# Kernel optimization log

Measured on AMD Instinct MI355X. Metric: run time of the kernel, lower is better.

The kernel has to match this reference:

```python
import jax, jax.numpy as jnp
import numpy as np

B, Cin, H, W = 4, 64, 160, 160
Cout, K, STRIDE, PAD = 64, 3, 1, 1
KK = K * K


def setup_inputs() -> dict:
    key = jax.random.key(0)
    ks = jax.random.split(key, 4)
    x = jax.random.normal(ks[0], (B, Cin, H, W), jnp.float32)
    # offset/mask conv params (zero-init in source; small random so offsets are non-trivial)
    offset_w = jax.random.normal(ks[1], (3 * KK, Cin, K, K), jnp.float32) * 0.01
    offset_b = jax.random.normal(ks[2], (3 * KK,), jnp.float32) * 0.01
    fan_in = Cin * K * K
    weight = jax.random.normal(ks[3], (Cout, Cin, K, K), jnp.float32) / np.sqrt(fan_in)
    bias = jnp.zeros((Cout,), jnp.float32)
    return dict(x=x, offset_w=offset_w, offset_b=offset_b, weight=weight, bias=bias)


def _conv2d(x, w, b):
    y = jax.lax.conv_general_dilated(
        x, w, window_strides=(STRIDE, STRIDE),
        padding=[(PAD, PAD), (PAD, PAD)],
        dimension_numbers=('NCHW', 'OIHW', 'NCHW'))
    return y + b[None, :, None, None]


def _deform_conv2d(x, offset, mask, weight, bias):
    # x: [B,C,H,W]; offset: [B,2*KK,Ho,Wo] as (dy,dx) pairs; mask: [B,KK,Ho,Wo]
    Bs, C, Hh, Ww = x.shape
    Ho, Wo = offset.shape[2], offset.shape[3]
    off = offset.reshape(Bs, KK, 2, Ho, Wo)
    dy, dx = off[:, :, 0], off[:, :, 1]            # [B,KK,Ho,Wo]
    ki, kj = jnp.meshgrid(jnp.arange(K), jnp.arange(K), indexing='ij')
    ki = ki.reshape(KK).astype(jnp.float32)
    kj = kj.reshape(KK).astype(jnp.float32)
    hb = (jnp.arange(Ho) * STRIDE - PAD).astype(jnp.float32)
    wb = (jnp.arange(Wo) * STRIDE - PAD).astype(jnp.float32)
    py = dy + ki[None, :, None, None] + hb[None, None, :, None]  # sample y coords
    px = dx + kj[None, :, None, None] + wb[None, None, None, :]  # sample x coords
    y0 = jnp.floor(py); x0 = jnp.floor(px)
    wy1 = py - y0; wy0 = 1.0 - wy1
    wx1 = px - x0; wx0 = 1.0 - wx1
    x_hwc = jnp.transpose(x, (0, 2, 3, 1))          # [B,H,W,C]

    def corner(yc, xc):
        valid = (yc >= 0) & (yc < Hh) & (xc >= 0) & (xc < Ww)
        yi = jnp.clip(yc, 0, Hh - 1).astype(jnp.int32)
        xi = jnp.clip(xc, 0, Ww - 1).astype(jnp.int32)
        g = jax.vmap(lambda img, yy, xx: img[yy, xx])(x_hwc, yi, xi)  # [B,KK,Ho,Wo,C]
        return g * valid[..., None].astype(x.dtype)

    val = (corner(y0, x0) * (wy0 * wx0)[..., None]
           + corner(y0, x0 + 1.0) * (wy0 * wx1)[..., None]
           + corner(y0 + 1.0, x0) * (wy1 * wx0)[..., None]
           + corner(y0 + 1.0, x0 + 1.0) * (wy1 * wx1)[..., None])
    val = val * mask[..., None]                      # modulated (DCNv2)
    w2 = weight.reshape(weight.shape[0], C, KK)      # [O,C,KK]
    out = jnp.einsum('bkhwc,ock->bohw', val, w2)
    return out + bias[None, :, None, None]


def reference(x, offset_w, offset_b, weight, bias):
    out = _conv2d(x, offset_w, offset_b)             # [B,3*KK,Ho,Wo]
    o1, o2, m = jnp.split(out, 3, axis=1)
    offset = jnp.concatenate([o1, o2], axis=1)       # [B,2*KK,Ho,Wo]
    mask = jax.nn.sigmoid(m)
    return _deform_conv2d(x, offset, mask, weight, bias)
```

## Files before the change

### kernel.cpp

```cpp
#include <hip/hip_runtime.h>
#include <hip/hip_bf16.h>
#include <math.h>

#define B_ 4
#define CIN 64
#define H_ 160
#define W_ 160
#define COUT 64
#define KK_ 9
#define HW_ (H_ * W_)
#define KTOT 576
#define APITCH 584
#define XPITCH 72
#define SLPITCH 17
#define NTILE 6400
#define TPX   800

typedef __attribute__((ext_vector_type(8))) short bf16x8;
typedef __attribute__((ext_vector_type(4))) float f32x4;

__device__ inline unsigned short f2bf(float f) {
    unsigned int u = __float_as_uint(f);
    u = (u + 0x7FFF + ((u >> 16) & 1)) >> 16;
    return (unsigned short)u;
}

__device__ inline unsigned short bfc(float f) {
    __hip_bfloat16 h = __float2bfloat16(f);
    union { __hip_bfloat16 h; unsigned short u; } cv;
    cv.h = h;
    return cv.u;
}

__global__ __launch_bounds__(256) void prep_all_k(const float* __restrict__ x,
                                                  const float* __restrict__ wgt,
                                                  const float* __restrict__ ow,
                                                  float* __restrict__ xt,
                                                  unsigned short* __restrict__ wB,
                                                  unsigned short* __restrict__ wB2) {
    __shared__ float tile[64][65];
    int bid = blockIdx.x;
    int t = threadIdx.x;

    if (bid < 1600) {
        int pbk = bid % 400, b = bid / 400;
        int p0 = pbk * 64;
        const float* xp = x + (size_t)b * CIN * HW_ + p0;

        int pg = (t & 15) * 4, cr = t >> 4;
#pragma unroll
        for (int i = 0; i < 4; i++) {
            int c = i * 16 + cr;
            float4 v = *(const float4*)(xp + (size_t)c * HW_ + pg);
            tile[c][pg]     = v.x;
            tile[c][pg + 1] = v.y;
            tile[c][pg + 2] = v.z;
            tile[c][pg + 3] = v.w;
        }
        __syncthreads();

        int c4 = (t & 15) * 4, pr = t >> 4;
        float* op = xt + ((size_t)b * HW_ + p0) * 64 + c4;
#pragma unroll
        for (int i = 0; i < 4; i++) {
            int p = i * 16 + pr;
            float4 v;
            v.x = tile[c4][p];
            v.y = tile[c4 + 1][p];
            v.z = tile[c4 + 2][p];
            v.w = tile[c4 + 3][p];
            *(float4*)(op + (size_t)p * 64) = v;
        }
    } else if (bid < 1744) {
        int i = (bid - 1600) * 256 + t;
        int o = i / KTOT, r = i % KTOT;
        int tap = r >> 6, c = r & 63;
        wB[i] = f2bf(wgt[(o * CIN + c) * KK_ + tap]);
    } else {
        int i = (bid - 1744) * 256 + t;
        int n = i / KTOT, r = i % KTOT;
        int tap = r >> 6, c = r & 63;
        wB2[i] = (n < 27) ? f2bf(ow[(n * CIN + c) * KK_ + tap]) : (unsigned short)0;
    }
}

__global__ __launch_bounds__(256, 6) void fused_dcn_k(const float* __restrict__ xt,
                                                      const unsigned short* __restrict__ wB2,
                                                      const float* __restrict__ ob,
                                                      const unsigned short* __restrict__ wB,
                                                      const float* __restrict__ bias,
                                                      float* __restrict__ out) {
    __shared__ __align__(16) char ubuf[16 * APITCH * 2];
    __shared__ __align__(16) char pbuf[144 * 32];
    __shared__ float slog[27 * SLPITCH];
    unsigned short* sX = (unsigned short*)ubuf;
    unsigned short* sA = (unsigned short*)ubuf;
    float4* spar_w = (float4*)pbuf;
    int4*   spar_o = (int4*)(pbuf + 144 * 16);

    int t = threadIdx.x;
    int lane = t & 63, wv = t >> 6;
    int bid = blockIdx.x;
    int tile = (bid & 7) * TPX + (bid >> 3);
    int gp0 = tile * 16;
    int wo0 = gp0 % W_;
    int tmp = gp0 / W_;
    int ho = tmp % H_;
    int b  = tmp / H_;

    const float* xb = xt + (size_t)b * HW_ * 64 + lane;

    for (int i = 0; i < 14; i++) {
        int r = i * 4 + wv;
        if (r < 54) {
            int yy = ho - 1 + r / 18;
            int xx = wo0 - 1 + r % 18;
            float v = 0.f;
            if (yy >= 0 && yy < H_ && xx >= 0 && xx < W_)
                v = xb[(size_t)(yy * W_ + xx) * 64];
            sX[r * XPITCH + lane] = bfc(v);
        }
    }
    __syncthreads();

    if (wv < 2) {
        int m = lane & 15, q = lane >> 4;
        int oc = wv * 16 + m;
        float bv = (oc < 27) ? ob[oc] : 0.f;
        f32x4 acc  = {bv, bv, bv, bv};
        f32x4 acc2 = {0.f, 0.f, 0.f, 0.f};
        const unsigned short* brow = wB2 + oc * KTOT + q * 8;
#pragma unroll
        for (int tap = 0; tap < 9; tap++) {
            int row = (tap / 3) * 18 + (tap % 3) + m;
            const unsigned short* sxr = sX + row * XPITCH + q * 8;
            bf16x8 af0 = *(const bf16x8*)(sxr);
            bf16x8 af1 = *(const bf16x8*)(sxr + 32);
            bf16x8 b0  = *(const bf16x8*)(brow + (2 * tap) * 32);
            bf16x8 b1  = *(const bf16x8*)(brow + (2 * tap + 1) * 32);
            acc  = __builtin_amdgcn_mfma_f32_16x16x32_bf16(af0, b0, acc,  0, 0, 0);
            acc2 = __builtin_amdgcn_mfma_f32_16x16x32_bf16(af1, b1, acc2, 0, 0, 0);
        }
#pragma unroll
        for (int r = 0; r < 4; r++) acc[r] += acc2[r];
        if (oc < 27) {
            float* sl = slog + oc * SLPITCH + q * 4;
            if (oc < 18) {
#pragma unroll
                for (int r = 0; r < 4; r++) sl[r] = acc[r];
            } else {
#pragma unroll
                for (int r = 0; r < 4; r++) sl[r] = 1.f / (1.f + expf(-acc[r]));
            }
        }
    }
    __syncthreads();

    if (lane < 36) {
        int task = lane * 4 + wv;
        int p = task & 15, k = task >> 4;
        float dyv = slog[(2 * k) * SLPITCH + p];
        float dxv = slog[(2 * k + 1) * SLPITCH + p];
        float mv  = slog[(18 + k) * SLPITCH + p];
        float py = dyv + (float)(k / 3) + (float)(ho - 1);
        float px = dxv + (float)(k % 3) + (float)(wo0 + p - 1);
        float y0f = floorf(py), x0f = floorf(px);
        float wy1 = py - y0f, wx1 = px - x0f;
        float wy0 = 1.f - wy1, wx0 = 1.f - wx1;
        int y0 = (int)y0f, x0 = (int)x0f;
        bool yv0 = (y0 >= 0) && (y0 < H_);
        bool yv1 = (y0 + 1 >= 0) && (y0 + 1 < H_);
        bool xv0 = (x0 >= 0) && (x0 < W_);
        bool xv1 = (x0 + 1 >= 0) && (x0 + 1 < W_);
        float4 w4;
        w4.x = (yv0 && xv0) ? wy0 * wx0 * mv : 0.f;
        w4.y = (yv0 && xv1) ? wy0 * wx1 * mv : 0.f;
        w4.z = (yv1 && xv0) ? wy1 * wx0 * mv : 0.f;
        w4.w = (yv1 && xv1) ? wy1 * wx1 * mv : 0.f;
        spar_w[task] = w4;
        int yc0 = min(max(y0, 0), H_ - 1), yc1 = min(max(y0 + 1, 0), H_ - 1);
        int xc0 = min(max(x0, 0), W_ - 1), xc1 = min(max(x0 + 1, 0), W_ - 1);
        int4 o4;
        o4.x = (yc0 * W_ + xc0) * 256;
        o4.y = (yc0 * W_ + xc1) * 256;
        o4.z = (yc1 * W_ + xc0) * 256;
        o4.w = (yc1 * W_ + xc1) * 256;
        spar_o[task] = o4;
    }
    __asm__ volatile("s_waitcnt lgkmcnt(0)" ::: "memory");

    {
        unsigned lane4 = (unsigned)lane << 2;
        const char* xu = (const char*)xt + (size_t)b * ((size_t)HW_ * 64 * 4);
#pragma unroll
        for (int g = 0; g < 6; g++) {
            float v00[6], v01[6], v10[6], v11[6];
#pragma unroll
            for (int j = 0; j < 6; j++) {
                int task = (g * 6 + j) * 4 + wv;
                int4 o4 = spar_o[task];
                v00[j] = *(const float*)(xu + ((unsigned)o4.x + lane4));
                v01[j] = *(const float*)(xu + ((unsigned)o4.y + lane4));
                v10[j] = *(const float*)(xu + ((unsigned)o4.z + lane4));
                v11[j] = *(const float*)(xu + ((unsigned)o4.w + lane4));
            }
#pragma unroll
            for (int j = 0; j < 6; j++) {
                int task = (g * 6 + j) * 4 + wv;
                float4 w4 = spar_w[task];
                int p = task & 15, k = task >> 4;
                float v = v00[j] * w4.x + v01[j] * w4.y
                        + v10[j] * w4.z + v11[j] * w4.w;
                sA[p * APITCH + k * 64 + lane] = bfc(v);
            }
        }
    }
    __syncthreads();

    int m = lane & 15, q = lane >> 4;
    int o0 = wv * 16 + m;
    float b0v = bias[o0];
    f32x4 acc0 = {b0v, b0v, b0v, b0v};
    f32x4 acc1 = {0.f, 0.f, 0.f, 0.f};
    const unsigned short* arow = sA + m * APITCH + q * 8;
    const unsigned short* br0 = wB + o0 * KTOT + q * 8;
#pragma unroll
    for (int tap = 0; tap < 9; tap++) {
        bf16x8 af0 = *(const bf16x8*)(arow + (2 * tap) * 32);
        bf16x8 af1 = *(const bf16x8*)(arow + (2 * tap + 1) * 32);
        bf16x8 b0  = *(const bf16x8*)(br0 + (2 * tap) * 32);
        bf16x8 b1  = *(const bf16x8*)(br0 + (2 * tap + 1) * 32);
        acc0 = __builtin_amdgcn_mfma_f32_16x16x32_bf16(af0, b0, acc0, 0, 0, 0);
        acc1 = __builtin_amdgcn_mfma_f32_16x16x32_bf16(af1, b1, acc1, 0, 0, 0);
    }
#pragma unroll
    for (int r = 0; r < 4; r++) acc0[r] += acc1[r];

    size_t a0 = ((size_t)(b * COUT + o0)) * HW_ + (size_t)ho * W_ + wo0 + q * 4;
    float4 r0; r0.x = acc0[0]; r0.y = acc0[1]; r0.z = acc0[2]; r0.w = acc0[3];
    *(float4*)(out + a0) = r0;
}

extern "C" void kernel_launch(void* const* d_in, const int* in_sizes, int n_in,
                              void* d_out, int out_size, void* d_ws, size_t ws_size,
                              hipStream_t stream) {
    const float* x    = (const float*)d_in[0];
    const float* ow   = (const float*)d_in[1];
    const float* ob   = (const float*)d_in[2];
    const float* wgt  = (const float*)d_in[3];
    const float* bias = (const float*)d_in[4];
    float* out = (float*)d_out;

    float* ws  = (float*)d_ws;
    float* xt  = ws;
    unsigned short* wB  = (unsigned short*)(xt + (size_t)B_ * HW_ * CIN);
    unsigned short* wB2 = wB + (size_t)COUT * KTOT;

    prep_all_k<<<1816, 256, 0, stream>>>(x, wgt, ow, xt, wB, wB2);
    fused_dcn_k<<<NTILE, 256, 0, stream>>>(xt, wB2, ob, wB, bias, out);
}
```

Measured before the change: 200.6 us.

## Stage a 5x20 fp32 input halo in LDS and gather bilinear corners from it

Each block loads a 5-row by 20-column fp32 halo of the input (all 64 channels) into shared memory and uses it to build the bf16 tile for the offset conv. Bilinear sample corners that fall inside this halo are read from LDS, and only out-of-window samples fall back to global gathers, flagged per task. The aim is to replace scattered global gathers with LDS reads, since offsets are small. In exchange, LDS use per block grows by about 25 KB and the launch-bounds occupancy hint drops from 6 to 3 blocks.

```diff
diff --git a/kernel.cpp b/kernel.cpp
--- a/kernel.cpp
+++ b/kernel.cpp
@@ -84,7 +84,7 @@
     }
 }
 
-__global__ __launch_bounds__(256, 6) void fused_dcn_k(const float* __restrict__ xt,
+__global__ __launch_bounds__(256, 3) void fused_dcn_k(const float* __restrict__ xt,
                                                       const unsigned short* __restrict__ wB2,
                                                       const float* __restrict__ ob,
                                                       const unsigned short* __restrict__ wB,
@@ -93,6 +93,8 @@
     __shared__ __align__(16) char ubuf[16 * APITCH * 2];
     __shared__ __align__(16) char pbuf[144 * 32];
     __shared__ float slog[27 * SLPITCH];
+    __shared__ unsigned sflag[144];
+    __shared__ __align__(16) float sF[100 * 64];
     unsigned short* sX = (unsigned short*)ubuf;
     unsigned short* sA = (unsigned short*)ubuf;
     float4* spar_w = (float4*)pbuf;
@@ -110,16 +112,18 @@
 
     const float* xb = xt + (size_t)b * HW_ * 64 + lane;
 
-    for (int i = 0; i < 14; i++) {
-        int r = i * 4 + wv;
-        if (r < 54) {
-            int yy = ho - 1 + r / 18;
-            int xx = wo0 - 1 + r % 18;
-            float v = 0.f;
-            if (yy >= 0 && yy < H_ && xx >= 0 && xx < W_)
-                v = xb[(size_t)(yy * W_ + xx) * 64];
-            sX[r * XPITCH + lane] = bfc(v);
-        }
+#pragma unroll
+    for (int i = 0; i < 25; i++) {
+        int p = i * 4 + wv;
+        int ry = p / 20, rx = p % 20;
+        int yy = ho - 2 + ry;
+        int xx = wo0 - 2 + rx;
+        float v = 0.f;
+        if (yy >= 0 && yy < H_ && xx >= 0 && xx < W_)
+            v = xb[(size_t)(yy * W_ + xx) * 64];
+        sF[p * 64 + lane] = v;
+        if (ry >= 1 && ry <= 3 && rx >= 1 && rx <= 18)
+            sX[((ry - 1) * 18 + (rx - 1)) * XPITCH + lane] = bfc(v);
     }
     __syncthreads();
 
@@ -180,38 +184,77 @@
         spar_w[task] = w4;
         int yc0 = min(max(y0, 0), H_ - 1), yc1 = min(max(y0 + 1, 0), H_ - 1);
         int xc0 = min(max(x0, 0), W_ - 1), xc1 = min(max(x0 + 1, 0), W_ - 1);
+        bool ins = (yc0 >= ho - 2) && (yc1 <= ho + 2) &&
+                   (xc0 >= wo0 - 2) && (xc1 <= wo0 + 17);
         int4 o4;
-        o4.x = (yc0 * W_ + xc0) * 256;
-        o4.y = (yc0 * W_ + xc1) * 256;
-        o4.z = (yc1 * W_ + xc0) * 256;
-        o4.w = (yc1 * W_ + xc1) * 256;
+        if (ins) {
+            int ry0 = yc0 - (ho - 2), ry1 = yc1 - (ho - 2);
+            int rx0 = xc0 - (wo0 - 2), rx1 = xc1 - (wo0 - 2);
+            o4.x = (ry0 * 20 + rx0) * 256;
+            o4.y = (ry0 * 20 + rx1) * 256;
+            o4.z = (ry1 * 20 + rx0) * 256;
+            o4.w = (ry1 * 20 + rx1) * 256;
+        } else {
+            o4.x = (yc0 * W_ + xc0) * 256;
+            o4.y = (yc0 * W_ + xc1) * 256;
+            o4.z = (yc1 * W_ + xc0) * 256;
+            o4.w = (yc1 * W_ + xc1) * 256;
+        }
         spar_o[task] = o4;
+        sflag[task] = ins ? 0u : 1u;
     }
     __asm__ volatile("s_waitcnt lgkmcnt(0)" ::: "memory");
 
     {
         unsigned lane4 = (unsigned)lane << 2;
-        const char* xu = (const char*)xt + (size_t)b * ((size_t)HW_ * 64 * 4);
+        const char* xu  = (const char*)xt + (size_t)b * ((size_t)HW_ * 64 * 4);
+        const char* sFb = (const char*)sF;
 #pragma unroll
         for (int g = 0; g < 6; g++) {
-            float v00[6], v01[6], v10[6], v11[6];
+            int4 o4[6]; float4 w4[6]; unsigned fl = 0;
 #pragma unroll
             for (int j = 0; j < 6; j++) {
                 int task = (g * 6 + j) * 4 + wv;
-                int4 o4 = spar_o[task];
-                v00[j] = *(const float*)(xu + ((unsigned)o4.x + lane4));
-                v01[j] = *(const float*)(xu + ((unsigned)o4.y + lane4));
-                v10[j] = *(const float*)(xu + ((unsigned)o4.z + lane4));
-                v11[j] = *(const float*)(xu + ((unsigned)o4.w + lane4));
+                o4[j] = spar_o[task];
+                w4[j] = spar_w[task];
+                fl |= sflag[task];
+            }
+            float v[6];
+            if (fl == 0) {
+#pragma unroll
+                for (int j = 0; j < 6; j++) {
+                    float v00 = *(const float*)(sFb + ((unsigned)o4[j].x + lane4));
+                    float v01 = *(const float*)(sFb + ((unsigned)o4[j].y + lane4));
+                    float v10 = *(const float*)(sFb + ((unsigned)o4[j].z + lane4));
+                    float v11 = *(const float*)(sFb + ((unsigned)o4[j].w + lane4));
+                    v[j] = v00 * w4[j].x + v01 * w4[j].y
+                         + v10 * w4[j].z + v11 * w4[j].w;
+                }
+            } else {
+#pragma unroll
+                for (int j = 0; j < 6; j++) {
+                    int task = (g * 6 + j) * 4 + wv;
+                    float v00, v01, v10, v11;
+                    if (sflag[task] == 0) {
+                        v00 = *(const float*)(sFb + ((unsigned)o4[j].x + lane4));
+                        v01 = *(const float*)(sFb + ((unsigned)o4[j].y + lane4));
+                        v10 = *(const float*)(sFb + ((unsigned)o4[j].z + lane4));
+                        v11 = *(const float*)(sFb + ((unsigned)o4[j].w + lane4));
+                    } else {
+                        v00 = *(const float*)(xu + ((unsigned)o4[j].x + lane4));
+                        v01 = *(const float*)(xu + ((unsigned)o4[j].y + lane4));
+                        v10 = *(const float*)(xu + ((unsigned)o4[j].z + lane4));
+                        v11 = *(const float*)(xu + ((unsigned)o4[j].w + lane4));
+                    }
+                    v[j] = v00 * w4[j].x + v01 * w4[j].y
+                         + v10 * w4[j].z + v11 * w4[j].w;
+                }
             }
 #pragma unroll
             for (int j = 0; j < 6; j++) {
                 int task = (g * 6 + j) * 4 + wv;
-                float4 w4 = spar_w[task];
                 int p = task & 15, k = task >> 4;
-                float v = v00[j] * w4.x + v01[j] * w4.y
-                        + v10[j] * w4.z + v11[j] * w4.w;
-                sA[p * APITCH + k * 64 + lane] = bfc(v);
+                sA[p * APITCH + k * 64 + lane] = bfc(v[j]);
             }
         }
     }
```

Result: slower. 234.4 us (+16.9%).

## Process four tiles per block with register prefetch of next halo

Applied to the files above, without the earlier changes.

Each block now loops over four consecutive 16-pixel tiles instead of one, reducing the grid from 6400 to 1600 blocks. The next tile's input halo is loaded into registers while the current tile's offset conv, sampling and GEMM run, hiding global load latency. This amortizes block launch overhead but adds register pressure, extra barriers per tile, and leaves fewer blocks for load balancing.

```diff
diff --git a/kernel.cpp b/kernel.cpp
--- a/kernel.cpp
+++ b/kernel.cpp
@@ -13,8 +13,8 @@
 #define APITCH 584
 #define XPITCH 72
 #define SLPITCH 17
-#define NTILE 6400
-#define TPX   800
+#define NBLK 1600
+#define SPX  200
 
 typedef __attribute__((ext_vector_type(8))) short bf16x8;
 typedef __attribute__((ext_vector_type(4))) float f32x4;
@@ -101,144 +101,180 @@
     int t = threadIdx.x;
     int lane = t & 63, wv = t >> 6;
     int bid = blockIdx.x;
-    int tile = (bid & 7) * TPX + (bid >> 3);
-    int gp0 = tile * 16;
-    int wo0 = gp0 % W_;
-    int tmp = gp0 / W_;
-    int ho = tmp % H_;
-    int b  = tmp / H_;
-
+    int s = (bid & 7) * SPX + (bid >> 3);
+    int b = s / 400;
     const float* xb = xt + (size_t)b * HW_ * 64 + lane;
 
-    for (int i = 0; i < 14; i++) {
-        int r = i * 4 + wv;
-        if (r < 54) {
-            int yy = ho - 1 + r / 18;
-            int xx = wo0 - 1 + r % 18;
+    float rp[14];
+    {
+        int gpP = (s * 4) * 16;
+        int woP = gpP % W_;
+        int hoP = (gpP / W_) % H_;
+#pragma unroll
+        for (int i = 0; i < 14; i++) {
+            int r = i * 4 + wv;
             float v = 0.f;
-            if (yy >= 0 && yy < H_ && xx >= 0 && xx < W_)
-                v = xb[(size_t)(yy * W_ + xx) * 64];
-            sX[r * XPITCH + lane] = bfc(v);
+            if (r < 54) {
+                int yy = hoP - 1 + r / 18;
+                int xx = woP - 1 + r % 18;
+                if (yy >= 0 && yy < H_ && xx >= 0 && xx < W_)
+                    v = xb[(size_t)(yy * W_ + xx) * 64];
+            }
+            rp[i] = v;
         }
     }
-    __syncthreads();
-
-    if (wv < 2) {
-        int m = lane & 15, q = lane >> 4;
-        int oc = wv * 16 + m;
-        float bv = (oc < 27) ? ob[oc] : 0.f;
-        f32x4 acc  = {bv, bv, bv, bv};
-        f32x4 acc2 = {0.f, 0.f, 0.f, 0.f};
-        const unsigned short* brow = wB2 + oc * KTOT + q * 8;
-#pragma unroll
-        for (int tap = 0; tap < 9; tap++) {
-            int row = (tap / 3) * 18 + (tap % 3) + m;
-            const unsigned short* sxr = sX + row * XPITCH + q * 8;
-            bf16x8 af0 = *(const bf16x8*)(sxr);
-            bf16x8 af1 = *(const bf16x8*)(sxr + 32);
-            bf16x8 b0  = *(const bf16x8*)(brow + (2 * tap) * 32);
-            bf16x8 b1  = *(const bf16x8*)(brow + (2 * tap + 1) * 32);
-            acc  = __builtin_amdgcn_mfma_f32_16x16x32_bf16(af0, b0, acc,  0, 0, 0);
-            acc2 = __builtin_amdgcn_mfma_f32_16x16x32_bf16(af1, b1, acc2, 0, 0, 0);
-        }
-#pragma unroll
-        for (int r = 0; r < 4; r++) acc[r] += acc2[r];
-        if (oc < 27) {
-            float* sl = slog + oc * SLPITCH + q * 4;
-            if (oc < 18) {
-#pragma unroll
-                for (int r = 0; r < 4; r++) sl[r] = acc[r];
-            } else {
-#pragma unroll
-                for (int r = 0; r < 4; r++) sl[r] = 1.f / (1.f + expf(-acc[r]));
-            }
-        }
+
+#pragma unroll
+    for (int ti = 0; ti < 4; ti++) {
+        int gp0 = (s * 4 + ti) * 16;
+        int wo0 = gp0 % W_;
+        int ho  = (gp0 / W_) % H_;
+
+#pragma unroll
+        for (int i = 0; i < 14; i++) {
+            int r = i * 4 + wv;
+            if (r < 54) sX[r * XPITCH + lane] = bfc(rp[i]);
+        }
+        __syncthreads();
+
+        if (ti < 3) {
+            int gpN = (s * 4 + ti + 1) * 16;
+            int woN = gpN % W_;
+            int hoN = (gpN / W_) % H_;
+#pragma unroll
+            for (int i = 0; i < 14; i++) {
+                int r = i * 4 + wv;
+                float v = 0.f;
+                if (r < 54) {
+                    int yy = hoN - 1 + r / 18;
+                    int xx = woN - 1 + r % 18;
+                    if (yy >= 0 && yy < H_ && xx >= 0 && xx < W_)
+                        v = xb[(size_t)(yy * W_ + xx) * 64];
+                }
+                rp[i] = v;
+            }
+        }
+
+        if (wv < 2) {
+            int m = lane & 15, q = lane >> 4;
+            int oc = wv * 16 + m;
+            float bv = (oc < 27) ? ob[oc] : 0.f;
+            f32x4 acc  = {bv, bv, bv, bv};
+            f32x4 acc2 = {0.f, 0.f, 0.f, 0.f};
+            const unsigned short* brow = wB2 + oc * KTOT + q * 8;
+#pragma unroll
+            for (int tap = 0; tap < 9; tap++) {
+                int row = (tap / 3) * 18 + (tap % 3) + m;
+                const unsigned short* sxr = sX + row * XPITCH + q * 8;
+                bf16x8 af0 = *(const bf16x8*)(sxr);
+                bf16x8 af1 = *(const bf16x8*)(sxr + 32);
+                bf16x8 b0  = *(const bf16x8*)(brow + (2 * tap) * 32);
+                bf16x8 b1  = *(const bf16x8*)(brow + (2 * tap + 1) * 32);
+                acc  = __builtin_amdgcn_mfma_f32_16x16x32_bf16(af0, b0, acc,  0, 0, 0);
+                acc2 = __builtin_amdgcn_mfma_f32_16x16x32_bf16(af1, b1, acc2, 0, 0, 0);
+            }
+#pragma unroll
+            for (int r = 0; r < 4; r++) acc[r] += acc2[r];
+            if (oc < 27) {
+                float* sl = slog + oc * SLPITCH + q * 4;
+                if (oc < 18) {
+#pragma unroll
+                    for (int r = 0; r < 4; r++) sl[r] = acc[r];
+                } else {
+#pragma unroll
+                    for (int r = 0; r < 4; r++) sl[r] = 1.f / (1.f + expf(-acc[r]));
+                }
+            }
+        }
+        __syncthreads();
+
+        if (lane < 36) {
+            int task = lane * 4 + wv;
+            int p = task & 15, k = task >> 4;
+            float dyv = slog[(2 * k) * SLPITCH + p];
+            float dxv = slog[(2 * k + 1) * SLPITCH + p];
+            float mv  = slog[(18 + k) * SLPITCH + p];
+            float py = dyv + (float)(k / 3) + (float)(ho - 1);
+            float px = dxv + (float)(k % 3) + (float)(wo0 + p - 1);
+            float y0f = floorf(py), x0f = floorf(px);
+            float wy1 = py - y0f, wx1 = px - x0f;
+            float wy0 = 1.f - wy1, wx0 = 1.f - wx1;
+            int y0 = (int)y0f, x0 = (int)x0f;
+            bool yv0 = (y0 >= 0) && (y0 < H_);
+            bool yv1 = (y0 + 1 >= 0) && (y0 + 1 < H_);
+            bool xv0 = (x0 >= 0) && (x0 < W_);
+            bool xv1 = (x0 + 1 >= 0) && (x0 + 1 < W_);
+            float4 w4;
+            w4.x = (yv0 && xv0) ? wy0 * wx0 * mv : 0.f;
+            w4.y = (yv0 && xv1) ? wy0 * wx1 * mv : 0.f;
+            w4.z = (yv1 && xv0) ? wy1 * wx0 * mv : 0.f;
+            w4.w = (yv1 && xv1) ? wy1 * wx1 * mv : 0.f;
+            spar_w[task] = w4;
+            int yc0 = min(max(y0, 0), H_ - 1), yc1 = min(max(y0 + 1, 0), H_ - 1);
+            int xc0 = min(max(x0, 0), W_ - 1), xc1 = min(max(x0 + 1, 0), W_ - 1);
+            int4 o4;
+            o4.x = (yc0 * W_ + xc0) * 256;
+            o4.y = (yc0 * W_ + xc1) * 256;
+            o4.z = (yc1 * W_ + xc0) * 256;
+            o4.w = (yc1 * W_ + xc1) * 256;
+            spar_o[task] = o4;
+        }
+        __asm__ volatile("s_waitcnt lgkmcnt(0)" ::: "memory");
+
+        {
+            unsigned lane4 = (unsigned)lane << 2;
+            const char* xu = (const char*)xt + (size_t)b * ((size_t)HW_ * 64 * 4);
+#pragma unroll
+            for (int g = 0; g < 6; g++) {
+                float v00[6], v01[6], v10[6], v11[6];
+#pragma unroll
+                for (int j = 0; j < 6; j++) {
+                    int task = (g * 6 + j) * 4 + wv;
+                    int4 o4 = spar_o[task];
+                    v00[j] = *(const float*)(xu + ((unsigned)o4.x + lane4));
+                    v01[j] = *(const float*)(xu + ((unsigned)o4.y + lane4));
+                    v10[j] = *(const float*)(xu + ((unsigned)o4.z + lane4));
+                    v11[j] = *(const float*)(xu + ((unsigned)o4.w + lane4));
+                }
+#pragma unroll
+                for (int j = 0; j < 6; j++) {
+                    int task = (g * 6 + j) * 4 + wv;
+                    float4 w4 = spar_w[task];
+                    int p = task & 15, k = task >> 4;
+                    float v = v00[j] * w4.x + v01[j] * w4.y
+                            + v10[j] * w4.z + v11[j] * w4.w;
+                    sA[p * APITCH + k * 64 + lane] = bfc(v);
+                }
+            }
+        }
+        __syncthreads();
+
+        {
+            int m = lane & 15, q = lane >> 4;
+            int o0 = wv * 16 + m;
+            float b0v = bias[o0];
+            f32x4 acc0 = {b0v, b0v, b0v, b0v};
+            f32x4 acc1 = {0.f, 0.f, 0.f, 0.f};
+            const unsigned short* arow = sA + m * APITCH + q * 8;
+            const unsigned short* br0 = wB + o0 * KTOT + q * 8;
+#pragma unroll
+            for (int tap = 0; tap < 9; tap++) {
+                bf16x8 af0 = *(const bf16x8*)(arow + (2 * tap) * 32);
+                bf16x8 af1 = *(const bf16x8*)(arow + (2 * tap + 1) * 32);
+                bf16x8 b0  = *(const bf16x8*)(br0 + (2 * tap) * 32);
+                bf16x8 b1  = *(const bf16x8*)(br0 + (2 * tap + 1) * 32);
+                acc0 = __builtin_amdgcn_mfma_f32_16x16x32_bf16(af0, b0, acc0, 0, 0, 0);
+                acc1 = __builtin_amdgcn_mfma_f32_16x16x32_bf16(af1, b1, acc1, 0, 0, 0);
+            }
+#pragma unroll
+            for (int r = 0; r < 4; r++) acc0[r] += acc1[r];
+
+            size_t a0 = ((size_t)(b * COUT + o0)) * HW_ + (size_t)ho * W_ + wo0 + q * 4;
+            float4 r0; r0.x = acc0[0]; r0.y = acc0[1]; r0.z = acc0[2]; r0.w = acc0[3];
+            *(float4*)(out + a0) = r0;
+        }
+        __syncthreads();
     }
-    __syncthreads();
-
-    if (lane < 36) {
-        int task = lane * 4 + wv;
-        int p = task & 15, k = task >> 4;
-        float dyv = slog[(2 * k) * SLPITCH + p];
-        float dxv = slog[(2 * k + 1) * SLPITCH + p];
-        float mv  = slog[(18 + k) * SLPITCH + p];
-        float py = dyv + (float)(k / 3) + (float)(ho - 1);
-        float px = dxv + (float)(k % 3) + (float)(wo0 + p - 1);
-        float y0f = floorf(py), x0f = floorf(px);
-        float wy1 = py - y0f, wx1 = px - x0f;
-        float wy0 = 1.f - wy1, wx0 = 1.f - wx1;
-        int y0 = (int)y0f, x0 = (int)x0f;
-        bool yv0 = (y0 >= 0) && (y0 < H_);
-        bool yv1 = (y0 + 1 >= 0) && (y0 + 1 < H_);
-        bool xv0 = (x0 >= 0) && (x0 < W_);
-        bool xv1 = (x0 + 1 >= 0) && (x0 + 1 < W_);
-        float4 w4;
-        w4.x = (yv0 && xv0) ? wy0 * wx0 * mv : 0.f;
-        w4.y = (yv0 && xv1) ? wy0 * wx1 * mv : 0.f;
-        w4.z = (yv1 && xv0) ? wy1 * wx0 * mv : 0.f;
-        w4.w = (yv1 && xv1) ? wy1 * wx1 * mv : 0.f;
-        spar_w[task] = w4;
-        int yc0 = min(max(y0, 0), H_ - 1), yc1 = min(max(y0 + 1, 0), H_ - 1);
-        int xc0 = min(max(x0, 0), W_ - 1), xc1 = min(max(x0 + 1, 0), W_ - 1);
-        int4 o4;
-        o4.x = (yc0 * W_ + xc0) * 256;
-        o4.y = (yc0 * W_ + xc1) * 256;
-        o4.z = (yc1 * W_ + xc0) * 256;
-        o4.w = (yc1 * W_ + xc1) * 256;
-        spar_o[task] = o4;
-    }
-    __asm__ volatile("s_waitcnt lgkmcnt(0)" ::: "memory");
-
-    {
-        unsigned lane4 = (unsigned)lane << 2;
-        const char* xu = (const char*)xt + (size_t)b * ((size_t)HW_ * 64 * 4);
-#pragma unroll
-        for (int g = 0; g < 6; g++) {
-            float v00[6], v01[6], v10[6], v11[6];
-#pragma unroll
-            for (int j = 0; j < 6; j++) {
-                int task = (g * 6 + j) * 4 + wv;
-                int4 o4 = spar_o[task];
-                v00[j] = *(const float*)(xu + ((unsigned)o4.x + lane4));
-                v01[j] = *(const float*)(xu + ((unsigned)o4.y + lane4));
-                v10[j] = *(const float*)(xu + ((unsigned)o4.z + lane4));
-                v11[j] = *(const float*)(xu + ((unsigned)o4.w + lane4));
-            }
-#pragma unroll
-            for (int j = 0; j < 6; j++) {
-                int task = (g * 6 + j) * 4 + wv;
-                float4 w4 = spar_w[task];
-                int p = task & 15, k = task >> 4;
-                float v = v00[j] * w4.x + v01[j] * w4.y
-                        + v10[j] * w4.z + v11[j] * w4.w;
-                sA[p * APITCH + k * 64 + lane] = bfc(v);
-            }
-        }
-    }
-    __syncthreads();
-
-    int m = lane & 15, q = lane >> 4;
-    int o0 = wv * 16 + m;
-    float b0v = bias[o0];
-    f32x4 acc0 = {b0v, b0v, b0v, b0v};
-    f32x4 acc1 = {0.f, 0.f, 0.f, 0.f};
-    const unsigned short* arow = sA + m * APITCH + q * 8;
-    const unsigned short* br0 = wB + o0 * KTOT + q * 8;
-#pragma unroll
-    for (int tap = 0; tap < 9; tap++) {
-        bf16x8 af0 = *(const bf16x8*)(arow + (2 * tap) * 32);
-        bf16x8 af1 = *(const bf16x8*)(arow + (2 * tap + 1) * 32);
-        bf16x8 b0  = *(const bf16x8*)(br0 + (2 * tap) * 32);
-        bf16x8 b1  = *(const bf16x8*)(br0 + (2 * tap + 1) * 32);
-        acc0 = __builtin_amdgcn_mfma_f32_16x16x32_bf16(af0, b0, acc0, 0, 0, 0);
-        acc1 = __builtin_amdgcn_mfma_f32_16x16x32_bf16(af1, b1, acc1, 0, 0, 0);
-    }
-#pragma unroll
-    for (int r = 0; r < 4; r++) acc0[r] += acc1[r];
-
-    size_t a0 = ((size_t)(b * COUT + o0)) * HW_ + (size_t)ho * W_ + wo0 + q * 4;
-    float4 r0; r0.x = acc0[0]; r0.y = acc0[1]; r0.z = acc0[2]; r0.w = acc0[3];
-    *(float4*)(out + a0) = r0;
 }
 
 extern "C" void kernel_launch(void* const* d_in, const int* in_sizes, int n_in,
@@ -257,5 +293,5 @@
     unsigned short* wB2 = wB + (size_t)COUT * KTOT;
 
     prep_all_k<<<1816, 256, 0, stream>>>(x, wgt, ow, xt, wB, wB2);
-    fused_dcn_k<<<NTILE, 256, 0, stream>>>(xt, wB2, ob, wB, bias, out);
-}
+    fused_dcn_k<<<NBLK, 256, 0, stream>>>(xt, wB2, ob, wB, bias, out);
+}
```

Result: slower. 258.4 us (+28.8%).

## Chunk im2col tile into three tap groups to shrink LDS and raise occupancy

Applied to the files above, without the earlier changes.

The bilinear-sampled A tile is no longer built for all 9 taps before the MFMA loop. It is now produced in three chunks of 3 taps each, and each chunk is consumed by MFMAs right away. This cuts the LDS A buffer from 16x584 to 16x200 bf16, and launch bounds rise from 6 to 8 waves per SIMD so more blocks can be resident. The cost is extra __syncthreads per block and tighter register limits, which could cause spills.

```diff
diff --git a/kernel.cpp b/kernel.cpp
--- a/kernel.cpp
+++ b/kernel.cpp
@@ -10,7 +10,7 @@
 #define KK_ 9
 #define HW_ (H_ * W_)
 #define KTOT 576
-#define APITCH 584
+#define CPITCH 200
 #define XPITCH 72
 #define SLPITCH 17
 #define NTILE 6400
@@ -84,17 +84,17 @@
     }
 }
 
-__global__ __launch_bounds__(256, 6) void fused_dcn_k(const float* __restrict__ xt,
+__global__ __launch_bounds__(256, 8) void fused_dcn_k(const float* __restrict__ xt,
                                                       const unsigned short* __restrict__ wB2,
                                                       const float* __restrict__ ob,
                                                       const unsigned short* __restrict__ wB,
                                                       const float* __restrict__ bias,
                                                       float* __restrict__ out) {
-    __shared__ __align__(16) char ubuf[16 * APITCH * 2];
+    __shared__ __align__(16) char ubuf[7776];
     __shared__ __align__(16) char pbuf[144 * 32];
     __shared__ float slog[27 * SLPITCH];
-    unsigned short* sX = (unsigned short*)ubuf;
-    unsigned short* sA = (unsigned short*)ubuf;
+    unsigned short* sX  = (unsigned short*)ubuf;
+    unsigned short* sAc = (unsigned short*)ubuf;
     float4* spar_w = (float4*)pbuf;
     int4*   spar_o = (int4*)(pbuf + 144 * 16);
 
@@ -189,15 +189,25 @@
     }
     __asm__ volatile("s_waitcnt lgkmcnt(0)" ::: "memory");
 
-    {
-        unsigned lane4 = (unsigned)lane << 2;
-        const char* xu = (const char*)xt + (size_t)b * ((size_t)HW_ * 64 * 4);
-#pragma unroll
-        for (int g = 0; g < 6; g++) {
+    int m = lane & 15, q = lane >> 4;
+    int o0 = wv * 16 + m;
+    float b0v = bias[o0];
+    f32x4 acc0 = {b0v, b0v, b0v, b0v};
+    f32x4 acc1 = {0.f, 0.f, 0.f, 0.f};
+    const unsigned short* br0 = wB + o0 * KTOT + q * 8;
+    const unsigned short* arow = sAc + m * CPITCH + q * 8;
+
+    unsigned lane4 = (unsigned)lane << 2;
+    const char* xu = (const char*)xt + (size_t)b * ((size_t)HW_ * 64 * 4);
+
+#pragma unroll
+    for (int c = 0; c < 3; c++) {
+#pragma unroll
+        for (int g = 0; g < 2; g++) {
             float v00[6], v01[6], v10[6], v11[6];
 #pragma unroll
             for (int j = 0; j < 6; j++) {
-                int task = (g * 6 + j) * 4 + wv;
+                int task = 48 * c + (g * 6 + j) * 4 + wv;
                 int4 o4 = spar_o[task];
                 v00[j] = *(const float*)(xu + ((unsigned)o4.x + lane4));
                 v01[j] = *(const float*)(xu + ((unsigned)o4.y + lane4));
@@ -206,33 +216,28 @@
             }
 #pragma unroll
             for (int j = 0; j < 6; j++) {
-                int task = (g * 6 + j) * 4 + wv;
+                int task = 48 * c + (g * 6 + j) * 4 + wv;
                 float4 w4 = spar_w[task];
-                int p = task & 15, k = task >> 4;
+                int p = task & 15, kc = (task >> 4) - 3 * c;
                 float v = v00[j] * w4.x + v01[j] * w4.y
                         + v10[j] * w4.z + v11[j] * w4.w;
-                sA[p * APITCH + k * 64 + lane] = bfc(v);
+                sAc[p * CPITCH + kc * 64 + lane] = bfc(v);
             }
         }
-    }
-    __syncthreads();
-
-    int m = lane & 15, q = lane >> 4;
-    int o0 = wv * 16 + m;
-    float b0v = bias[o0];
-    f32x4 acc0 = {b0v, b0v, b0v, b0v};
-    f32x4 acc1 = {0.f, 0.f, 0.f, 0.f};
-    const unsigned short* arow = sA + m * APITCH + q * 8;
-    const unsigned short* br0 = wB + o0 * KTOT + q * 8;
-#pragma unroll
-    for (int tap = 0; tap < 9; tap++) {
-        bf16x8 af0 = *(const bf16x8*)(arow + (2 * tap) * 32);
-        bf16x8 af1 = *(const bf16x8*)(arow + (2 * tap + 1) * 32);
-        bf16x8 b0  = *(const bf16x8*)(br0 + (2 * tap) * 32);
-        bf16x8 b1  = *(const bf16x8*)(br0 + (2 * tap + 1) * 32);
-        acc0 = __builtin_amdgcn_mfma_f32_16x16x32_bf16(af0, b0, acc0, 0, 0, 0);
-        acc1 = __builtin_amdgcn_mfma_f32_16x16x32_bf16(af1, b1, acc1, 0, 0, 0);
-    }
+        __syncthreads();
+
+#pragma unroll
+        for (int tl = 0; tl < 3; tl++) {
+            bf16x8 af0 = *(const bf16x8*)(arow + (2 * tl) * 32);
+            bf16x8 af1 = *(const bf16x8*)(arow + (2 * tl + 1) * 32);
+            bf16x8 b0  = *(const bf16x8*)(br0 + ((c * 3 + tl) * 2) * 32);
+            bf16x8 b1  = *(const bf16x8*)(br0 + ((c * 3 + tl) * 2 + 1) * 32);
+            acc0 = __builtin_amdgcn_mfma_f32_16x16x32_bf16(af0, b0, acc0, 0, 0, 0);
+            acc1 = __builtin_amdgcn_mfma_f32_16x16x32_bf16(af1, b1, acc1, 0, 0, 0);
+        }
+        if (c < 2) __syncthreads();
+    }
+
 #pragma unroll
     for (int r = 0; r < 4; r++) acc0[r] += acc1[r];
 
```

Result: no change. 198.3 us (-1.1%).
